# Kernel optimization log

Hardware: AMD Instinct MI355X
Metric: run time of the kernel (lower is better)

Reference implementation:

```python
import jax, jax.numpy as jnp
import numpy as np

D_MODEL = 1024
NUM_HEADS = 16
DEPTH = D_MODEL // NUM_HEADS
B, S = 8, 1024


def setup_inputs() -> dict:
    key = jax.random.key(0)
    ks = jax.random.split(key, 12)
    sc = 0.02
    return {
        "v": jax.random.normal(ks[0], (B, S, D_MODEL), jnp.float32),
        "k": jax.random.normal(ks[1], (B, S, D_MODEL), jnp.float32),
        "q_in": jax.random.normal(ks[2], (B, S, D_MODEL), jnp.float32),
        "mask": jnp.zeros((B, 1, 1, S), jnp.float32),
        "wq_w": jax.random.normal(ks[3], (D_MODEL, D_MODEL), jnp.float32) * sc,
        "wq_b": jnp.zeros((D_MODEL,), jnp.float32),
        "wk_w": jax.random.normal(ks[4], (D_MODEL, D_MODEL), jnp.float32) * sc,
        "wk_b": jnp.zeros((D_MODEL,), jnp.float32),
        "wv_w": jax.random.normal(ks[5], (D_MODEL, D_MODEL), jnp.float32) * sc,
        "wv_b": jnp.zeros((D_MODEL,), jnp.float32),
        "wo_w": jax.random.normal(ks[6], (2 * D_MODEL, D_MODEL), jnp.float32) * sc,
        "wo_b": jnp.zeros((D_MODEL,), jnp.float32),
    }


def _split_heads(x):
    # (B, S, D) -> (B, H, S, depth)
    b, s, _ = x.shape
    return x.reshape(b, s, NUM_HEADS, DEPTH).transpose(0, 2, 1, 3)


def reference(v, k, q_in, mask, wq_w, wq_b, wk_w, wk_b, wv_w, wv_b, wo_w, wo_b):
    q = _split_heads(q_in @ wq_w + wq_b)   # (B,H,Sq,depth)
    kk = _split_heads(k @ wk_w + wk_b)     # (B,H,Sk,depth)
    vv = _split_heads(v @ wv_w + wv_b)     # (B,H,Sk,depth)

    scale = 1.0 / jnp.sqrt(jnp.float32(DEPTH))
    logits = jnp.einsum("bhqd,bhkd->bhqk", q, kk) * scale
    logits = logits + mask * (-1e9)
    attn = jax.nn.softmax(logits, axis=-1)  # dropout inactive (inference)
    ctx = jnp.einsum("bhqk,bhkd->bhqd", attn, vv)

    # (B,H,Sq,depth) -> (B,Sq,D)
    ctx = ctx.transpose(0, 2, 1, 3).reshape(q_in.shape[0], -1, D_MODEL)
    concat = jnp.concatenate([q_in, ctx], axis=-1)  # (B,Sq,2D)
    out = concat @ wo_w + wo_b
    return out
```

## Files before the change

### kernel.cpp

```cpp
#include <hip/hip_runtime.h>

#define NHEADS 16
#define DEPTH  64
#define BATCH  8
#define SEQ    1024
#define DMODEL 1024
#define MTOT   (BATCH*SEQ)

typedef float f32x4 __attribute__((ext_vector_type(4)));
typedef int   i32x4 __attribute__((ext_vector_type(4)));
typedef unsigned short u16;

static __device__ inline u16 f2bf(float x) {
    unsigned int u = __builtin_bit_cast(unsigned int, x);
    u += 0x7FFFu + ((u >> 16) & 1u);
    return (u16)(u >> 16);
}

static __device__ inline unsigned cvt_pk_bf16(float lo, float hi) {
    unsigned r;
    asm("v_cvt_pk_bf16_f32 %0, %1, %2" : "=v"(r) : "v"(lo), "v"(hi));
    return r;
}

static __device__ inline void mfma_bf16(f32x4& acc, i32x4 a, i32x4 b) {
    asm("v_mfma_f32_16x16x32_bf16 %0, %1, %2, %0" : "+v"(acc) : "v"(a), "v"(b));
}

static __device__ inline void gload16(const u16* g, u16* l) {
    __builtin_amdgcn_global_load_lds(
        (const __attribute__((address_space(1))) void*)g,
        (__attribute__((address_space(3))) void*)l,
        16, 0, 0);
}

__global__ __launch_bounds__(256) void cvt_kernel(
    const float* __restrict__ A, const float* __restrict__ B, const float* __restrict__ C,
    u16* __restrict__ Ao, u16* __restrict__ Bo, u16* __restrict__ Co)
{
    const float* src = (blockIdx.y == 0) ? A : (blockIdx.y == 1) ? B : C;
    u16* dst         = (blockIdx.y == 0) ? Ao : (blockIdx.y == 1) ? Bo : Co;
    int i = (blockIdx.x * 256 + threadIdx.x) * 8;
    float4 f0 = *reinterpret_cast<const float4*>(src + i);
    float4 f1 = *reinterpret_cast<const float4*>(src + i + 4);
    uint4 u;
    u.x = cvt_pk_bf16(f0.x, f0.y);
    u.y = cvt_pk_bf16(f0.z, f0.w);
    u.z = cvt_pk_bf16(f1.x, f1.y);
    u.w = cvt_pk_bf16(f1.z, f1.w);
    *reinterpret_cast<uint4*>(dst + i) = u;
}

__global__ __launch_bounds__(256) void transpose_cvt_kernel(
    const float* __restrict__ W, u16* __restrict__ Wt, int K, int N)
{
    __shared__ u16 tile[32][33];
    int n0 = blockIdx.x * 32, k0 = blockIdx.y * 32;
    int tx = threadIdx.x & 31, ty = threadIdx.x >> 5;
    #pragma unroll
    for (int r = 0; r < 32; r += 8)
        tile[r + ty][tx] = f2bf(W[(k0 + r + ty) * N + n0 + tx]);
    __syncthreads();
    #pragma unroll
    for (int r = 0; r < 32; r += 8)
        Wt[(n0 + r + ty) * K + k0 + tx] = tile[tx][r + ty];
}

__global__ __launch_bounds__(256) void proj_kernel(
    const u16* __restrict__ Xq, const u16* __restrict__ Xk, const u16* __restrict__ Xv,
    const u16* __restrict__ Wtq, const u16* __restrict__ Wtk, const u16* __restrict__ Wtv,
    const float* __restrict__ Bq, const float* __restrict__ Bk, const float* __restrict__ Bv,
    u16* __restrict__ Qh, u16* __restrict__ Kh, u16* __restrict__ Vt)
{
    const int z = blockIdx.z;
    const u16* X    = (z == 0) ? Xq  : (z == 1) ? Xk  : Xv;
    const u16* Wt   = (z == 0) ? Wtq : (z == 1) ? Wtk : Wtv;
    const float* Bi = (z == 0) ? Bq  : (z == 1) ? Bk  : Bv;
    u16* Out        = (z == 0) ? Qh  : (z == 1) ? Kh  : Vt;

    __shared__ u16 As[128 * 64];
    __shared__ u16 Bs[128 * 64];

    const int t = threadIdx.x;
    const int m0 = blockIdx.x * 128, n0 = blockIdx.y * 128;
    const int lane = t & 63, w = t >> 6;
    const int wu = __builtin_amdgcn_readfirstlane(w);
    const int wm = w >> 1, wn = w & 1;
    const int lr = lane & 15, lg = lane >> 4;
    const int srow = lane >> 3;
    const int scol = ((lane & 7) ^ (srow & 7)) * 8;

    const u16* ga = X  + (m0 + wu * 32 + srow) * DMODEL + scol;
    const u16* gb = Wt + (n0 + wu * 32 + srow) * DMODEL + scol;
    u16* la = As + wu * 32 * 64;
    u16* lb = Bs + wu * 32 * 64;

    f32x4 acc[4][4];
    #pragma unroll
    for (int i = 0; i < 4; ++i)
        #pragma unroll
        for (int j = 0; j < 4; ++j) acc[i][j] = f32x4{0.f, 0.f, 0.f, 0.f};

    for (int k0 = 0; k0 < DMODEL; k0 += 64) {
        __syncthreads();
        gload16(ga + k0,               la);
        gload16(ga + k0 +  8 * DMODEL, la +  8 * 64);
        gload16(ga + k0 + 16 * DMODEL, la + 16 * 64);
        gload16(ga + k0 + 24 * DMODEL, la + 24 * 64);
        gload16(gb + k0,               lb);
        gload16(gb + k0 +  8 * DMODEL, lb +  8 * 64);
        gload16(gb + k0 + 16 * DMODEL, lb + 16 * 64);
        gload16(gb + k0 + 24 * DMODEL, lb + 24 * 64);
        __syncthreads();
        #pragma unroll
        for (int kk = 0; kk < 2; ++kk) {
            const int pslot = ((kk * 4 + lg) ^ (lr & 7)) << 3;
            i32x4 af[4], bfr[4];
            #pragma unroll
            for (int mi = 0; mi < 4; ++mi)
                af[mi] = *reinterpret_cast<const i32x4*>(
                    &As[(wm * 64 + mi * 16 + lr) * 64 + pslot]);
            #pragma unroll
            for (int ni = 0; ni < 4; ++ni)
                bfr[ni] = *reinterpret_cast<const i32x4*>(
                    &Bs[(wn * 64 + ni * 16 + lr) * 64 + pslot]);
            #pragma unroll
            for (int mi = 0; mi < 4; ++mi)
                #pragma unroll
                for (int ni = 0; ni < 4; ++ni)
                    mfma_bf16(acc[mi][ni], af[mi], bfr[ni]);
        }
    }
    asm volatile("s_nop 7\n\ts_nop 7");
    #pragma unroll
    for (int mi = 0; mi < 4; ++mi)
        #pragma unroll
        for (int ni = 0; ni < 4; ++ni) {
            int n = n0 + wn * 64 + ni * 16 + lr;
            float bv = Bi[n];
            int h = n >> 6, d = n & 63;
            int mb = m0 + wm * 64 + mi * 16 + lg * 4;
            int b = mb >> 10, srw = mb & 1023;
            if (z == 2) {
                uint2 u;
                u.x = cvt_pk_bf16(acc[mi][ni][0] + bv, acc[mi][ni][1] + bv);
                u.y = cvt_pk_bf16(acc[mi][ni][2] + bv, acc[mi][ni][3] + bv);
                *reinterpret_cast<uint2*>(&Vt[(((b << 4) + h) * DEPTH + d) * SEQ + srw]) = u;
            } else if (z == 0) {
                #pragma unroll
                for (int r = 0; r < 4; ++r)
                    Out[(((b << 4) + h) * SEQ + srw + r) * DEPTH + d] = f2bf((acc[mi][ni][r] + bv) * 0.18033688f);
            } else {
                #pragma unroll
                for (int r = 0; r < 4; ++r)
                    Out[(((b << 4) + h) * SEQ + srw + r) * DEPTH + d] = f2bf(acc[mi][ni][r] + bv);
            }
        }
}

__global__ __launch_bounds__(256) void attn_kernel(
    const u16* __restrict__ Qh, const u16* __restrict__ Kh, const u16* __restrict__ Vt,
    const float* __restrict__ mask, u16* __restrict__ CTX)
{
    __shared__ u16 Ks[64 * 64];
    __shared__ u16 Vts[64 * 64];
    __shared__ u16 Ps[4][32 * 64];
    __shared__ float Ms[SEQ];

    const int t = threadIdx.x;
    const int lane = t & 63, w = t >> 6;
    const int lr = lane & 15, lg = lane >> 4;
    const int bh = blockIdx.y;
    const int b = bh >> 4, h = bh & 15;
    const int qw = blockIdx.x * 128 + w * 32;

    const u16* Qp = Qh + bh * (SEQ * DEPTH);
    const u16* Kp = Kh + bh * (SEQ * DEPTH);
    const u16* Vp = Vt + bh * (SEQ * DEPTH);

    {
        float4 mv = *reinterpret_cast<const float4*>(mask + b * SEQ + t * 4);
        const float mk = -1.4426950408889634e9f;
        Ms[t * 4 + 0] = mv.x * mk;
        Ms[t * 4 + 1] = mv.y * mk;
        Ms[t * 4 + 2] = mv.z * mk;
        Ms[t * 4 + 3] = mv.w * mk;
    }

    i32x4 aq[2][2];
    #pragma unroll
    for (int g = 0; g < 2; ++g) {
        aq[g][0] = *reinterpret_cast<const i32x4*>(&Qp[(qw + g * 16 + lr) * DEPTH + lg * 8]);
        aq[g][1] = *reinterpret_cast<const i32x4*>(&Qp[(qw + g * 16 + lr) * DEPTH + 32 + lg * 8]);
    }

    f32x4 ctx[2][4];
    #pragma unroll
    for (int g = 0; g < 2; ++g)
        #pragma unroll
        for (int i = 0; i < 4; ++i) ctx[g][i] = f32x4{0.f, 0.f, 0.f, 0.f};
    float psum[2] = {0.f, 0.f};

    const int r0 = t >> 3;
    const int c8 = t & 7;
    const int swz0 = (c8 ^ (r0 & 7)) * 8;
    u16* kd0 = Ks  + r0 * 64 + swz0;
    u16* kd1 = Ks  + (r0 + 32) * 64 + swz0;
    u16* vd0 = Vts + r0 * 64 + swz0;
    u16* vd1 = Vts + (r0 + 32) * 64 + swz0;
    const u16* ksrc0 = Kp + r0 * DEPTH + c8 * 8;
    const u16* ksrc1 = Kp + (r0 + 32) * DEPTH + c8 * 8;
    const u16* vsrc0 = Vp + r0 * SEQ + c8 * 8;
    const u16* vsrc1 = Vp + (r0 + 32) * SEQ + c8 * 8;
    u16* PsW = Ps[w];

    u16* pdst[2][4];
    #pragma unroll
    for (int g = 0; g < 2; ++g)
        #pragma unroll
        for (int tt = 0; tt < 4; ++tt) {
            int slot = tt * 2 + (lg >> 1);
            pdst[g][tt] = PsW + (g * 16 + lr) * 64 + ((slot ^ (lr & 7)) << 3) + ((lg & 1) << 2);
        }

    uint4 kr0 = *reinterpret_cast<const uint4*>(ksrc0);
    uint4 kr1 = *reinterpret_cast<const uint4*>(ksrc1);
    uint4 vr0 = *reinterpret_cast<const uint4*>(vsrc0);
    uint4 vr1 = *reinterpret_cast<const uint4*>(vsrc1);

    for (int kt = 0; kt < SEQ; kt += 64) {
        __syncthreads();
        *reinterpret_cast<uint4*>(kd0) = kr0;
        *reinterpret_cast<uint4*>(kd1) = kr1;
        *reinterpret_cast<uint4*>(vd0) = vr0;
        *reinterpret_cast<uint4*>(vd1) = vr1;
        if (kt + 64 < SEQ) {
            int kn = kt + 64;
            kr0 = *reinterpret_cast<const uint4*>(ksrc0 + kn * DEPTH);
            kr1 = *reinterpret_cast<const uint4*>(ksrc1 + kn * DEPTH);
            vr0 = *reinterpret_cast<const uint4*>(vsrc0 + kn);
            vr1 = *reinterpret_cast<const uint4*>(vsrc1 + kn);
        }
        __syncthreads();

        f32x4 sc[2][4];
        #pragma unroll
        for (int g = 0; g < 2; ++g)
            #pragma unroll
            for (int i = 0; i < 4; ++i) sc[g][i] = f32x4{0.f, 0.f, 0.f, 0.f};
        #pragma unroll
        for (int tt = 0; tt < 4; ++tt) {
            int row = tt * 16 + lr, rs = row & 7;
            const u16* kr = Ks + row * 64;
            i32x4 bk0 = *reinterpret_cast<const i32x4*>(kr + ((lg ^ rs) << 3));
            i32x4 bk1 = *reinterpret_cast<const i32x4*>(kr + (((4 + lg) ^ rs) << 3));
            mfma_bf16(sc[0][tt], bk0, aq[0][0]);
            mfma_bf16(sc[0][tt], bk1, aq[0][1]);
            mfma_bf16(sc[1][tt], bk0, aq[1][0]);
            mfma_bf16(sc[1][tt], bk1, aq[1][1]);
        }
        asm volatile("s_nop 7\n\ts_nop 7");

        #pragma unroll
        for (int tt = 0; tt < 4; ++tt) {
            float4 m4 = *reinterpret_cast<const float4*>(&Ms[kt + tt * 16 + lg * 4]);
            #pragma unroll
            for (int g = 0; g < 2; ++g) {
                float p0 = __builtin_amdgcn_exp2f(sc[g][tt][0] + m4.x);
                float p1 = __builtin_amdgcn_exp2f(sc[g][tt][1] + m4.y);
                float p2 = __builtin_amdgcn_exp2f(sc[g][tt][2] + m4.z);
                float p3 = __builtin_amdgcn_exp2f(sc[g][tt][3] + m4.w);
                psum[g] += (p0 + p1) + (p2 + p3);
                uint2 u;
                u.x = cvt_pk_bf16(p0, p1);
                u.y = cvt_pk_bf16(p2, p3);
                *reinterpret_cast<uint2*>(pdst[g][tt]) = u;
            }
        }

        const int rswz = lr & 7;
        i32x4 pa[2][2];
        #pragma unroll
        for (int g = 0; g < 2; ++g) {
            const u16* pr = PsW + (g * 16 + lr) * 64;
            pa[g][0] = *reinterpret_cast<const i32x4*>(pr + ((lg ^ rswz) << 3));
            pa[g][1] = *reinterpret_cast<const i32x4*>(pr + (((4 + lg) ^ rswz) << 3));
        }
        #pragma unroll
        for (int dt = 0; dt < 4; ++dt) {
            int dcol = dt * 16 + lr, ds = dcol & 7;
            const u16* vr = Vts + dcol * 64;
            i32x4 bv0 = *reinterpret_cast<const i32x4*>(vr + ((lg ^ ds) << 3));
            i32x4 bv1 = *reinterpret_cast<const i32x4*>(vr + (((4 + lg) ^ ds) << 3));
            mfma_bf16(ctx[0][dt], pa[0][0], bv0);
            mfma_bf16(ctx[0][dt], pa[0][1], bv1);
            mfma_bf16(ctx[1][dt], pa[1][0], bv0);
            mfma_bf16(ctx[1][dt], pa[1][1], bv1);
        }
    }
    asm volatile("s_nop 7\n\ts_nop 7");
    #pragma unroll
    for (int g = 0; g < 2; ++g) {
        psum[g] += __shfl_xor(psum[g], 16);
        psum[g] += __shfl_xor(psum[g], 32);
    }
    float inv0 = 1.f / psum[0];
    float inv1 = 1.f / psum[1];
    #pragma unroll
    for (int g = 0; g < 2; ++g) {
        float invr[4];
        #pragma unroll
        for (int r = 0; r < 4; ++r)
            invr[r] = __shfl(g ? inv1 : inv0, lg * 4 + r);
        #pragma unroll
        for (int dt = 0; dt < 4; ++dt)
            #pragma unroll
            for (int r = 0; r < 4; ++r) {
                int s = qw + g * 16 + lg * 4 + r;
                int d = dt * 16 + lr;
                CTX[(b * SEQ + s) * DMODEL + h * DEPTH + d] = f2bf(ctx[g][dt][r] * invr[r]);
            }
    }
}

__global__ __launch_bounds__(256) void outproj_kernel(
    const float* __restrict__ Xq, const u16* __restrict__ CTX,
    const u16* __restrict__ Wto,
    const float* __restrict__ Bo, float* __restrict__ Out)
{
    __shared__ u16 As[128 * 64];
    __shared__ u16 Bs[128 * 64];

    const int t = threadIdx.x;
    const int m0 = blockIdx.x * 128, n0 = blockIdx.y * 128;
    const int lane = t & 63, w = t >> 6;
    const int wu = __builtin_amdgcn_readfirstlane(w);
    const int wm = w >> 1, wn = w & 1;
    const int lr = lane & 15, lg = lane >> 4;
    const int srow = lane >> 3;
    const int scol = ((lane & 7) ^ (srow & 7)) * 8;

    const int arow = t >> 1, ahalf = t & 1;

    const u16* gac = CTX + (m0 + wu * 32 + srow) * DMODEL + scol;
    const u16* gb  = Wto + (n0 + wu * 32 + srow) * (2 * DMODEL) + scol;
    u16* la = As + wu * 32 * 64;
    u16* lb = Bs + wu * 32 * 64;

    f32x4 acc[4][4];
    #pragma unroll
    for (int i = 0; i < 4; ++i)
        #pragma unroll
        for (int j = 0; j < 4; ++j) acc[i][j] = f32x4{0.f, 0.f, 0.f, 0.f};

    for (int k0 = 0; k0 < 2 * DMODEL; k0 += 64) {
        __syncthreads();
        gload16(gb + k0,                      lb);
        gload16(gb + k0 +  8 * 2 * DMODEL,    lb +  8 * 64);
        gload16(gb + k0 + 16 * 2 * DMODEL,    lb + 16 * 64);
        gload16(gb + k0 + 24 * 2 * DMODEL,    lb + 24 * 64);
        if (k0 < DMODEL) {
            const float* s = Xq + (m0 + arow) * DMODEL + k0 + ahalf * 32;
            #pragma unroll
            for (int j = 0; j < 4; ++j) {
                float4 fa = *reinterpret_cast<const float4*>(s + j * 8);
                float4 fb = *reinterpret_cast<const float4*>(s + j * 8 + 4);
                uint4 u;
                u.x = cvt_pk_bf16(fa.x, fa.y);
                u.y = cvt_pk_bf16(fa.z, fa.w);
                u.z = cvt_pk_bf16(fb.x, fb.y);
                u.w = cvt_pk_bf16(fb.z, fb.w);
                int slot = ahalf * 4 + j;
                *reinterpret_cast<uint4*>(&As[arow * 64 + ((slot ^ (arow & 7)) << 3)]) = u;
            }
        } else {
            int kc = k0 - DMODEL;
            gload16(gac + kc,               la);
            gload16(gac + kc +  8 * DMODEL, la +  8 * 64);
            gload16(gac + kc + 16 * DMODEL, la + 16 * 64);
            gload16(gac + kc + 24 * DMODEL, la + 24 * 64);
        }
        __syncthreads();
        #pragma unroll
        for (int kk = 0; kk < 2; ++kk) {
            const int pslot = ((kk * 4 + lg) ^ (lr & 7)) << 3;
            i32x4 af[4], bfr[4];
            #pragma unroll
            for (int mi = 0; mi < 4; ++mi)
                af[mi] = *reinterpret_cast<const i32x4*>(
                    &As[(wm * 64 + mi * 16 + lr) * 64 + pslot]);
            #pragma unroll
            for (int ni = 0; ni < 4; ++ni)
                bfr[ni] = *reinterpret_cast<const i32x4*>(
                    &Bs[(wn * 64 + ni * 16 + lr) * 64 + pslot]);
            #pragma unroll
            for (int mi = 0; mi < 4; ++mi)
                #pragma unroll
                for (int ni = 0; ni < 4; ++ni)
                    mfma_bf16(acc[mi][ni], af[mi], bfr[ni]);
        }
    }
    asm volatile("s_nop 7\n\ts_nop 7");
    #pragma unroll
    for (int mi = 0; mi < 4; ++mi)
        #pragma unroll
        for (int ni = 0; ni < 4; ++ni) {
            int n = n0 + wn * 64 + ni * 16 + lr;
            float bv = Bo[n];
            #pragma unroll
            for (int r = 0; r < 4; ++r) {
                int m = m0 + wm * 64 + mi * 16 + lg * 4 + r;
                Out[m * DMODEL + n] = acc[mi][ni][r] + bv;
            }
        }
}

extern "C" void kernel_launch(void* const* d_in, const int* in_sizes, int n_in,
                              void* d_out, int out_size, void* d_ws, size_t ws_size,
                              hipStream_t stream) {
    const float* v    = (const float*)d_in[0];
    const float* k    = (const float*)d_in[1];
    const float* q_in = (const float*)d_in[2];
    const float* mask = (const float*)d_in[3];
    const float* wq_w = (const float*)d_in[4];
    const float* wq_b = (const float*)d_in[5];
    const float* wk_w = (const float*)d_in[6];
    const float* wk_b = (const float*)d_in[7];
    const float* wv_w = (const float*)d_in[8];
    const float* wv_b = (const float*)d_in[9];
    const float* wo_w = (const float*)d_in[10];
    const float* wo_b = (const float*)d_in[11];
    float* out = (float*)d_out;

    u16* ws  = (u16*)d_ws;
    u16* Wtq = ws;
    u16* Wtk = Wtq + (1u << 20);
    u16* Wtv = Wtk + (1u << 20);
    u16* Wto = Wtv + (1u << 20);
    u16* Qh  = Wto + (2u << 20);
    u16* Kh  = Qh + (8u << 20);
    u16* Vt  = Kh + (8u << 20);
    u16* CTX = Vt + (8u << 20);

    u16* Xbq = CTX;
    u16* Xbk = (u16*)d_out;
    u16* Xbv = (u16*)d_out + (8u << 20);

    cvt_kernel<<<dim3(4096, 3), 256, 0, stream>>>(q_in, k, v, Xbq, Xbk, Xbv);

    transpose_cvt_kernel<<<dim3(32, 32), 256, 0, stream>>>(wq_w, Wtq, 1024, 1024);
    transpose_cvt_kernel<<<dim3(32, 32), 256, 0, stream>>>(wk_w, Wtk, 1024, 1024);
    transpose_cvt_kernel<<<dim3(32, 32), 256, 0, stream>>>(wv_w, Wtv, 1024, 1024);
    transpose_cvt_kernel<<<dim3(32, 64), 256, 0, stream>>>(wo_w, Wto, 2048, 1024);

    proj_kernel<<<dim3(64, 8, 3), 256, 0, stream>>>(
        Xbq, Xbk, Xbv, Wtq, Wtk, Wtv, wq_b, wk_b, wv_b, Qh, Kh, Vt);

    attn_kernel<<<dim3(8, 128), 256, 0, stream>>>(Qh, Kh, Vt, mask, CTX);

    outproj_kernel<<<dim3(64, 8), 256, 0, stream>>>(q_in, CTX, Wto, wo_b, out);
}
```

Measured before the change: 204.5 us.

## Double-buffer outproj LDS, reuse bf16 q_in, write ctx head-major into Qh

The output projection now double-buffers its A/B tiles in shared memory and issues the next stage's loads before computing the current one, so each k-step needs one barrier instead of two. The q_in half of the A operand now comes from the bf16 copy made by cvt_kernel, so the fp32 reload and in-loop conversion are gone. The attention kernel writes its context in place over Q in head-major layout, and outproj reads it per head with a 64-element row stride. This frees the separate CTX buffer and keeps Xbq alive, at the cost of doubling LDS use (64KB per block), which may lower occupancy.

```diff
diff --git a/kernel.cpp b/kernel.cpp
--- a/kernel.cpp
+++ b/kernel.cpp
@@ -159,8 +159,8 @@
 }
 
 __global__ __launch_bounds__(256) void attn_kernel(
-    const u16* __restrict__ Qh, const u16* __restrict__ Kh, const u16* __restrict__ Vt,
-    const float* __restrict__ mask, u16* __restrict__ CTX)
+    u16* __restrict__ Qh, const u16* __restrict__ Kh, const u16* __restrict__ Vt,
+    const float* __restrict__ mask)
 {
     __shared__ u16 Ks[64 * 64];
     __shared__ u16 Vts[64 * 64];
@@ -171,10 +171,10 @@
     const int lane = t & 63, w = t >> 6;
     const int lr = lane & 15, lg = lane >> 4;
     const int bh = blockIdx.y;
-    const int b = bh >> 4, h = bh & 15;
+    const int b = bh >> 4;
     const int qw = blockIdx.x * 128 + w * 32;
 
-    const u16* Qp = Qh + bh * (SEQ * DEPTH);
+    u16* Qp       = Qh + bh * (SEQ * DEPTH);
     const u16* Kp = Kh + bh * (SEQ * DEPTH);
     const u16* Vp = Vt + bh * (SEQ * DEPTH);
 
@@ -318,18 +318,18 @@
             for (int r = 0; r < 4; ++r) {
                 int s = qw + g * 16 + lg * 4 + r;
                 int d = dt * 16 + lr;
-                CTX[(b * SEQ + s) * DMODEL + h * DEPTH + d] = f2bf(ctx[g][dt][r] * invr[r]);
+                Qp[s * DEPTH + d] = f2bf(ctx[g][dt][r] * invr[r]);
             }
     }
 }
 
 __global__ __launch_bounds__(256) void outproj_kernel(
-    const float* __restrict__ Xq, const u16* __restrict__ CTX,
+    const u16* __restrict__ Xbq, const u16* __restrict__ CTXh,
     const u16* __restrict__ Wto,
     const float* __restrict__ Bo, float* __restrict__ Out)
 {
-    __shared__ u16 As[128 * 64];
-    __shared__ u16 Bs[128 * 64];
+    __shared__ u16 As[2][128 * 64];
+    __shared__ u16 Bs[2][128 * 64];
 
     const int t = threadIdx.x;
     const int m0 = blockIdx.x * 128, n0 = blockIdx.y * 128;
@@ -340,12 +340,10 @@
     const int srow = lane >> 3;
     const int scol = ((lane & 7) ^ (srow & 7)) * 8;
 
-    const int arow = t >> 1, ahalf = t & 1;
-
-    const u16* gac = CTX + (m0 + wu * 32 + srow) * DMODEL + scol;
+    const int rowslab = m0 + wu * 32;
+    const int bb = rowslab >> 10, sr = rowslab & 1023;
+    const u16* gaq = Xbq + (rowslab + srow) * DMODEL + scol;
     const u16* gb  = Wto + (n0 + wu * 32 + srow) * (2 * DMODEL) + scol;
-    u16* la = As + wu * 32 * 64;
-    u16* lb = Bs + wu * 32 * 64;
 
     f32x4 acc[4][4];
     #pragma unroll
@@ -353,34 +351,36 @@
         #pragma unroll
         for (int j = 0; j < 4; ++j) acc[i][j] = f32x4{0.f, 0.f, 0.f, 0.f};
 
-    for (int k0 = 0; k0 < 2 * DMODEL; k0 += 64) {
-        __syncthreads();
-        gload16(gb + k0,                      lb);
-        gload16(gb + k0 +  8 * 2 * DMODEL,    lb +  8 * 64);
-        gload16(gb + k0 + 16 * 2 * DMODEL,    lb + 16 * 64);
-        gload16(gb + k0 + 24 * 2 * DMODEL,    lb + 24 * 64);
+    auto STAGE = [&](int buf, int k0) {
+        u16* la = As[buf] + wu * 32 * 64;
+        u16* lb = Bs[buf] + wu * 32 * 64;
+        gload16(gb + k0,                   lb);
+        gload16(gb + k0 +  8 * 2 * DMODEL, lb +  8 * 64);
+        gload16(gb + k0 + 16 * 2 * DMODEL, lb + 16 * 64);
+        gload16(gb + k0 + 24 * 2 * DMODEL, lb + 24 * 64);
+        const u16* ga;
+        int rstride;
         if (k0 < DMODEL) {
-            const float* s = Xq + (m0 + arow) * DMODEL + k0 + ahalf * 32;
-            #pragma unroll
-            for (int j = 0; j < 4; ++j) {
-                float4 fa = *reinterpret_cast<const float4*>(s + j * 8);
-                float4 fb = *reinterpret_cast<const float4*>(s + j * 8 + 4);
-                uint4 u;
-                u.x = cvt_pk_bf16(fa.x, fa.y);
-                u.y = cvt_pk_bf16(fa.z, fa.w);
-                u.z = cvt_pk_bf16(fb.x, fb.y);
-                u.w = cvt_pk_bf16(fb.z, fb.w);
-                int slot = ahalf * 4 + j;
-                *reinterpret_cast<uint4*>(&As[arow * 64 + ((slot ^ (arow & 7)) << 3)]) = u;
-            }
+            ga = gaq + k0;
+            rstride = DMODEL;
         } else {
-            int kc = k0 - DMODEL;
-            gload16(gac + kc,               la);
-            gload16(gac + kc +  8 * DMODEL, la +  8 * 64);
-            gload16(gac + kc + 16 * DMODEL, la + 16 * 64);
-            gload16(gac + kc + 24 * DMODEL, la + 24 * 64);
-        }
-        __syncthreads();
+            int h = (k0 - DMODEL) >> 6;
+            ga = CTXh + (((bb << 4) + h) * SEQ + sr + srow) * DEPTH + scol;
+            rstride = DEPTH;
+        }
+        gload16(ga,                la);
+        gload16(ga +  8 * rstride, la +  8 * 64);
+        gload16(ga + 16 * rstride, la + 16 * 64);
+        gload16(ga + 24 * rstride, la + 24 * 64);
+    };
+
+    STAGE(0, 0);
+    __syncthreads();
+    for (int ts = 0; ts < 32; ++ts) {
+        if (ts < 31) STAGE((ts + 1) & 1, (ts + 1) * 64);
+        const int cur = ts & 1;
+        const u16* Ac = As[cur];
+        const u16* Bc = Bs[cur];
         #pragma unroll
         for (int kk = 0; kk < 2; ++kk) {
             const int pslot = ((kk * 4 + lg) ^ (lr & 7)) << 3;
@@ -388,17 +388,18 @@
             #pragma unroll
             for (int mi = 0; mi < 4; ++mi)
                 af[mi] = *reinterpret_cast<const i32x4*>(
-                    &As[(wm * 64 + mi * 16 + lr) * 64 + pslot]);
+                    &Ac[(wm * 64 + mi * 16 + lr) * 64 + pslot]);
             #pragma unroll
             for (int ni = 0; ni < 4; ++ni)
                 bfr[ni] = *reinterpret_cast<const i32x4*>(
-                    &Bs[(wn * 64 + ni * 16 + lr) * 64 + pslot]);
+                    &Bc[(wn * 64 + ni * 16 + lr) * 64 + pslot]);
             #pragma unroll
             for (int mi = 0; mi < 4; ++mi)
                 #pragma unroll
                 for (int ni = 0; ni < 4; ++ni)
                     mfma_bf16(acc[mi][ni], af[mi], bfr[ni]);
         }
+        __syncthreads();
     }
     asm volatile("s_nop 7\n\ts_nop 7");
     #pragma unroll
@@ -440,9 +441,8 @@
     u16* Qh  = Wto + (2u << 20);
     u16* Kh  = Qh + (8u << 20);
     u16* Vt  = Kh + (8u << 20);
-    u16* CTX = Vt + (8u << 20);
-
-    u16* Xbq = CTX;
+    u16* Xbq = Vt + (8u << 20);
+
     u16* Xbk = (u16*)d_out;
     u16* Xbv = (u16*)d_out + (8u << 20);
 
@@ -456,7 +456,7 @@
     proj_kernel<<<dim3(64, 8, 3), 256, 0, stream>>>(
         Xbq, Xbk, Xbv, Wtq, Wtk, Wtv, wq_b, wk_b, wv_b, Qh, Kh, Vt);
 
-    attn_kernel<<<dim3(8, 128), 256, 0, stream>>>(Qh, Kh, Vt, mask, CTX);
-
-    outproj_kernel<<<dim3(64, 8), 256, 0, stream>>>(q_in, CTX, Wto, wo_b, out);
-}
+    attn_kernel<<<dim3(8, 128), 256, 0, stream>>>(Qh, Kh, Vt, mask);
+
+    outproj_kernel<<<dim3(64, 8), 256, 0, stream>>>(Xbq, Qh, Wto, wo_b, out);
+}
```

New measurement: 178.9 us. 12.5% less time.
